# Kernel optimization log

Measured on AMD Instinct MI355X. Metric: run time of the kernel, lower is better.

Reference implementation:

```python
import jax, jax.numpy as jnp
import numpy as np

NUM_HEADS = 16
D_K = 64  # d_model // num_heads = 1024 // 16


def setup_inputs() -> dict:
    key = jax.random.key(0)
    ks = jax.random.split(key, 5)
    b, s, d = 2, 2048, 1024
    scale = 0.02
    return {
        "x": jax.random.normal(ks[0], (b, s, d), dtype=jnp.float32),
        "W_qkv": jax.random.normal(ks[1], (d, 3 * d), dtype=jnp.float32) * scale,
        "b_qkv": jax.random.normal(ks[2], (3 * d,), dtype=jnp.float32) * scale,
        "W_o": jax.random.normal(ks[3], (d, d), dtype=jnp.float32) * scale,
        "b_o": jax.random.normal(ks[4], (d,), dtype=jnp.float32) * scale,
    }


def reference(x, W_qkv, b_qkv, W_o, b_o):
    b, s, d = x.shape
    h, dk = NUM_HEADS, D_K
    # fused QKV projection: (b, s, 3*d_model)
    qkv = x @ W_qkv + b_qkv
    # faithful to the torch rearrange 'b s (h d)' with d = 3*d_k, then chunk:
    # each head's contiguous 3*d_k slice is split into q, k, v.
    qkv = qkv.reshape(b, s, h, 3 * dk).transpose(0, 2, 1, 3)  # (b, h, s, 3*dk)
    q, k, v = jnp.split(qkv, 3, axis=-1)  # each (b, h, s, dk)
    inv_scale = 1.0 / np.float32(np.sqrt(dk))
    scores = jnp.einsum("bhqd,bhkd->bhqk", q, k) * inv_scale  # (b, h, s, s)
    attn = jax.nn.softmax(scores, axis=-1)
    ctx = jnp.einsum("bhqk,bhkd->bhqd", attn, v)  # (b, h, s, dk)
    ctx = ctx.transpose(0, 2, 1, 3).reshape(b, s, d)  # (b, s, d_model)
    return ctx @ W_o + b_o
```

## Files before the change

kernel.cpp:

```cpp
#include <hip/hip_runtime.h>
#include <hip/hip_bf16.h>
#include <stdint.h>

#define NHEADS 16
#define DKH    64
#define BB     2
#define SS     2048
#define DM     1024
#define MROWS  (BB * SS)

typedef __attribute__((ext_vector_type(8))) short bf8_t;
typedef __attribute__((ext_vector_type(4))) float f4_t;
typedef unsigned short u16;
typedef uint32_t u32;

__device__ __forceinline__ u16 f2bf(float f) {
    union { float f; u32 u; } v; v.f = f;
    return (u16)((v.u + 0x7fffu + ((v.u >> 16) & 1u)) >> 16);
}

__device__ __forceinline__ float fexp2(float x) {
#if __has_builtin(__builtin_amdgcn_exp2f)
    return __builtin_amdgcn_exp2f(x);
#else
    return __expf(x * 0.69314718056f);
#endif
}

__device__ __forceinline__ void async_copy16(void* lds, const void* g) {
    __builtin_amdgcn_global_load_lds(
        (__attribute__((address_space(1))) void*)(void*)g,
        (__attribute__((address_space(3))) void*)lds, 16, 0, 0);
}

#define MFMA32(a, b, c) __builtin_amdgcn_mfma_f32_16x16x32_bf16(a, b, c, 0, 0, 0)

__global__ void k_cvt(const float* __restrict__ in, u16* __restrict__ out, int n4) {
    int stride = gridDim.x * blockDim.x;
    for (int i = blockIdx.x * blockDim.x + threadIdx.x; i < n4; i += stride) {
        float4 v = ((const float4*)in)[i];
        ushort4 o;
        o.x = f2bf(v.x); o.y = f2bf(v.y); o.z = f2bf(v.z); o.w = f2bf(v.w);
        ((ushort4*)out)[i] = o;
    }
}

__global__ void k_transpose(const float* __restrict__ W, u16* __restrict__ Wt, int K, int N) {
    __shared__ float tile[32][33];
    int n0 = blockIdx.x * 32, k0 = blockIdx.y * 32;
    int tx = threadIdx.x & 31, ty = threadIdx.x >> 5;
    #pragma unroll
    for (int r = ty; r < 32; r += 8)
        tile[r][tx] = W[(size_t)(k0 + r) * N + n0 + tx];
    __syncthreads();
    #pragma unroll
    for (int r = ty; r < 32; r += 8)
        Wt[(size_t)(n0 + r) * K + k0 + tx] = f2bf(tile[tx][r]);
}

template<int MODE>
__global__ __launch_bounds__(256) void k_gemm(
    const u16* __restrict__ A, const u16* __restrict__ Bt,
    const float* __restrict__ bias,
    u16* __restrict__ q_out, u16* __restrict__ k_out, u16* __restrict__ vt_out,
    float* __restrict__ f_out,
    int N, int K)
{
    __shared__ u16 As[128 * 32];
    __shared__ u16 Bs[128 * 32];
    const int m0 = blockIdx.y * 128, n0 = blockIdx.x * 128;
    const int tid = threadIdx.x;
    const int w = tid >> 6, l = tid & 63;
    const int lr = l >> 2, lc = (l & 3) * 8;
    const int fr = l & 15, fk = (l >> 4) * 8;
    const int wm = (w >> 1) * 64, wn = (w & 1) * 64;
    f4_t acc[4][4] = {};

    for (int kt = 0; kt < K; kt += 32) {
        #pragma unroll
        for (int cc = 0; cc < 2; ++cc) {
            const int c = w + cc * 4;
            async_copy16(As + c * 512, A  + (size_t)(m0 + c * 16 + lr) * K + kt + lc);
            async_copy16(Bs + c * 512, Bt + (size_t)(n0 + c * 16 + lr) * K + kt + lc);
        }
        __syncthreads();
        bf8_t af[4], bfr[4];
        #pragma unroll
        for (int mf = 0; mf < 4; ++mf)
            af[mf] = *(const bf8_t*)&As[(wm + mf * 16 + fr) * 32 + fk];
        #pragma unroll
        for (int nf = 0; nf < 4; ++nf)
            bfr[nf] = *(const bf8_t*)&Bs[(wn + nf * 16 + fr) * 32 + fk];
        #pragma unroll
        for (int mf = 0; mf < 4; ++mf)
            #pragma unroll
            for (int nf = 0; nf < 4; ++nf)
                acc[mf][nf] = MFMA32(af[mf], bfr[nf], acc[mf][nf]);
        __syncthreads();
    }

    #pragma unroll
    for (int mf = 0; mf < 4; ++mf)
      #pragma unroll
      for (int nf = 0; nf < 4; ++nf)
        #pragma unroll
        for (int j = 0; j < 4; ++j) {
            const int m = m0 + wm + mf * 16 + (l >> 4) * 4 + j;
            const int n = n0 + wn + nf * 16 + (l & 15);
            float v = acc[mf][nf][j] + bias[n];
            if (MODE == 0) {
                const int h = n / 192, rem = n - h * 192;
                const int which = rem >> 6, dd = rem & 63;
                const int b = m >> 11, s = m & (SS - 1);
                const u16 bv = f2bf(v);
                const size_t qk_idx = ((size_t)(b * NHEADS + h) * SS + s) * DKH + dd;
                if (which == 0)      q_out[qk_idx] = bv;
                else if (which == 1) k_out[qk_idx] = bv;
                else                 vt_out[((size_t)(b * NHEADS + h) * DKH + dd) * SS + s] = bv;
            } else {
                f_out[(size_t)m * N + n] = v;
            }
        }
}

#define SCL 0.180336880f

__global__ __launch_bounds__(256) void k_attn(
    const u16* __restrict__ Qg, const u16* __restrict__ Kg, const u16* __restrict__ Vtg,
    u16* __restrict__ ctx)
{
    __shared__ u16 Ks[64 * 64];
    __shared__ u16 Vs[64 * 64];
    const int bh = blockIdx.x;
    const int qt = blockIdx.y;
    const int tid = threadIdx.x, w = tid >> 6, l = tid & 63;
    const int fr = l & 15, fq = l >> 4;
    const int q0 = qt * 64 + w * 16;
    const u16* Qb = Qg  + (size_t)bh * SS * DKH;
    const u16* Kb = Kg  + (size_t)bh * SS * DKH;
    const u16* Vb = Vtg + (size_t)bh * DKH * SS;

    bf8_t qf[2];
    #pragma unroll
    for (int kh = 0; kh < 2; ++kh)
        qf[kh] = *(const bf8_t*)(Qb + (size_t)(q0 + fr) * DKH + kh * 32 + fq * 8);

    float mrow = -__builtin_inff(), lrow = 0.f;
    f4_t o[4] = {};

    for (int kv = 0; kv < SS; kv += 64) {
        #pragma unroll
        for (int it = 0; it < 2; ++it) {
            const int c = tid + it * 256;
            const int r = c >> 3, sl = c & 7;
            const int dsl = sl ^ (r & 7);
            *(uint4*)&Ks[r * 64 + dsl * 8] = *(const uint4*)(Kb + (size_t)(kv + r) * DKH + sl * 8);
            *(uint4*)&Vs[r * 64 + dsl * 8] = *(const uint4*)(Vb + (size_t)r * SS + kv + sl * 8);
        }
        __syncthreads();

        f4_t sa[4] = {};
        #pragma unroll
        for (int nf = 0; nf < 4; ++nf)
          #pragma unroll
          for (int kh = 0; kh < 2; ++kh) {
            const int row = nf * 16 + fr;
            const int dsl = (kh * 4 + fq) ^ (fr & 7);
            const bf8_t kb = *(const bf8_t*)&Ks[row * 64 + dsl * 8];
            sa[nf] = MFMA32(kb, qf[kh], sa[nf]);
          }

        float x = sa[0][0];
        #pragma unroll
        for (int nf = 0; nf < 4; ++nf)
          #pragma unroll
          for (int j = 0; j < 4; ++j)
            x = fmaxf(x, sa[nf][j]);
        x *= SCL;
        x = fmaxf(x, __shfl_xor(x, 16));
        x = fmaxf(x, __shfl_xor(x, 32));

        if (__any(x > mrow + 8.f)) {
            float mnew = fmaxf(mrow, x);
            float sc = fexp2(mrow - mnew);
            lrow *= sc;
            mrow = mnew;
            float sc4[4];
            #pragma unroll
            for (int j = 0; j < 4; ++j) sc4[j] = __shfl(sc, fq * 4 + j);
            #pragma unroll
            for (int df = 0; df < 4; ++df)
              #pragma unroll
              for (int j = 0; j < 4; ++j)
                o[df][j] *= sc4[j];
        }

        float ps = 0.f;
        u32 pk[8];
        #pragma unroll
        for (int nf = 0; nf < 4; ++nf) {
            float p0 = fexp2(sa[nf][0] * SCL - mrow);
            float p1 = fexp2(sa[nf][1] * SCL - mrow);
            float p2 = fexp2(sa[nf][2] * SCL - mrow);
            float p3 = fexp2(sa[nf][3] * SCL - mrow);
            ps += (p0 + p1) + (p2 + p3);
            pk[nf * 2 + 0] = ((u32)f2bf(p1) << 16) | f2bf(p0);
            pk[nf * 2 + 1] = ((u32)f2bf(p3) << 16) | f2bf(p2);
        }
        ps += __shfl_xor(ps, 16);
        ps += __shfl_xor(ps, 32);
        lrow += ps;

        union { bf8_t v; u32 u[4]; } pa[2];
        #pragma unroll
        for (int t = 0; t < 2; ++t) {
            pa[t].u[0] = pk[4 * t + 0]; pa[t].u[1] = pk[4 * t + 1];
            pa[t].u[2] = pk[4 * t + 2]; pa[t].u[3] = pk[4 * t + 3];
        }
        #pragma unroll
        for (int t = 0; t < 2; ++t) {
            const int dslA = ((4 * t)     + (fq >> 1)) ^ (fr & 7);
            const int dslB = ((4 * t + 2) + (fq >> 1)) ^ (fr & 7);
            const int hoff = (fq & 1) * 4;
            #pragma unroll
            for (int df = 0; df < 4; ++df) {
                const int row = df * 16 + fr;
                union { bf8_t v; uint2 u[2]; } vv;
                vv.u[0] = *(const uint2*)&Vs[row * 64 + dslA * 8 + hoff];
                vv.u[1] = *(const uint2*)&Vs[row * 64 + dslB * 8 + hoff];
                o[df] = MFMA32(pa[t].v, vv.v, o[df]);
            }
        }
        __syncthreads();
    }

    float ml[4];
    #pragma unroll
    for (int j = 0; j < 4; ++j) ml[j] = __shfl(lrow, fq * 4 + j);

    const int b = bh >> 4, h = bh & 15;
    #pragma unroll
    for (int df = 0; df < 4; ++df)
      #pragma unroll
      for (int j = 0; j < 4; ++j) {
        const int s = q0 + fq * 4 + j;
        const int dd = df * 16 + fr;
        float v = o[df][j] / ml[j];
        ctx[((size_t)(b * SS + s)) * DM + h * DKH + dd] = f2bf(v);
      }
}

extern "C" void kernel_launch(void* const* d_in, const int* in_sizes, int n_in,
                              void* d_out, int out_size, void* d_ws, size_t ws_size,
                              hipStream_t stream)
{
    const float* x     = (const float*)d_in[0];
    const float* W_qkv = (const float*)d_in[1];
    const float* b_qkv = (const float*)d_in[2];
    const float* W_o   = (const float*)d_in[3];
    const float* b_o   = (const float*)d_in[4];
    float* out = (float*)d_out;

    char* ws = (char*)d_ws;
    u16* xb   = (u16*)(ws);
    u16* Wqkt = (u16*)(ws + 8388608);
    u16* Wot  = (u16*)(ws + 8388608 + 6291456);
    u16* Qg   = (u16*)(ws + 16777216);
    u16* Kg   = Qg  + 4194304;
    u16* Vtg  = Kg  + 4194304;
    u16* ctx  = xb;

    k_cvt<<<1024, 256, 0, stream>>>(x, xb, (MROWS * DM) / 4);
    k_transpose<<<dim3(3 * DM / 32, DM / 32), 256, 0, stream>>>(W_qkv, Wqkt, DM, 3 * DM);
    k_transpose<<<dim3(DM / 32, DM / 32), 256, 0, stream>>>(W_o, Wot, DM, DM);
    k_gemm<0><<<dim3(3 * DM / 128, MROWS / 128), 256, 0, stream>>>(
        xb, Wqkt, b_qkv, Qg, Kg, Vtg, nullptr, 3 * DM, DM);
    k_attn<<<dim3(BB * NHEADS, SS / 64), 256, 0, stream>>>(Qg, Kg, Vtg, ctx);
    k_gemm<1><<<dim3(DM / 128, MROWS / 128), 256, 0, stream>>>(
        ctx, Wot, b_o, nullptr, nullptr, nullptr, out, DM, DM);
}
```

Baseline: 230.1 us.

## Async global-to-LDS K/V loads with permuted rows, packed bf16 convert, wide V reads

Measured after the change: 226.7 us. About the same (-1.5%).

```diff
diff --git a/kernel.cpp b/kernel.cpp
--- a/kernel.cpp
+++ b/kernel.cpp
@@ -17,6 +17,12 @@
 __device__ __forceinline__ u16 f2bf(float f) {
     union { float f; u32 u; } v; v.f = f;
     return (u16)((v.u + 0x7fffu + ((v.u >> 16) & 1u)) >> 16);
+}
+
+__device__ __forceinline__ u32 cvt_pk_bf16(float lo, float hi) {
+    u32 r;
+    asm("v_cvt_pk_bf16_f32 %0, %1, %2" : "=v"(r) : "v"(lo), "v"(hi));
+    return r;
 }
 
 __device__ __forceinline__ float fexp2(float x) {
@@ -152,10 +158,12 @@
         #pragma unroll
         for (int it = 0; it < 2; ++it) {
             const int c = tid + it * 256;
-            const int r = c >> 3, sl = c & 7;
-            const int dsl = sl ^ (r & 7);
-            *(uint4*)&Ks[r * 64 + dsl * 8] = *(const uint4*)(Kb + (size_t)(kv + r) * DKH + sl * 8);
-            *(uint4*)&Vs[r * 64 + dsl * 8] = *(const uint4*)(Vb + (size_t)r * SS + kv + sl * 8);
+            const int r = c >> 3, dslw = c & 7;
+            const int sl = dslw ^ (r & 7);
+            const int sr = ((r >> 2) & 3) * 16 + (r >> 4) * 4 + (r & 3);
+            const int cb = it * 256 + w * 64;
+            async_copy16(Ks + cb * 8, Kb + (size_t)(kv + sr) * DKH + sl * 8);
+            async_copy16(Vs + cb * 8, Vb + (size_t)r * SS + kv + sl * 8);
         }
         __syncthreads();
 
@@ -204,8 +212,8 @@
             float p2 = fexp2(sa[nf][2] * SCL - mrow);
             float p3 = fexp2(sa[nf][3] * SCL - mrow);
             ps += (p0 + p1) + (p2 + p3);
-            pk[nf * 2 + 0] = ((u32)f2bf(p1) << 16) | f2bf(p0);
-            pk[nf * 2 + 1] = ((u32)f2bf(p3) << 16) | f2bf(p2);
+            pk[nf * 2 + 0] = cvt_pk_bf16(p0, p1);
+            pk[nf * 2 + 1] = cvt_pk_bf16(p2, p3);
         }
         ps += __shfl_xor(ps, 16);
         ps += __shfl_xor(ps, 32);
@@ -219,16 +227,11 @@
         }
         #pragma unroll
         for (int t = 0; t < 2; ++t) {
-            const int dslA = ((4 * t)     + (fq >> 1)) ^ (fr & 7);
-            const int dslB = ((4 * t + 2) + (fq >> 1)) ^ (fr & 7);
-            const int hoff = (fq & 1) * 4;
+            const int dsl = (fq * 2 + t) ^ (fr & 7);
             #pragma unroll
             for (int df = 0; df < 4; ++df) {
-                const int row = df * 16 + fr;
-                union { bf8_t v; uint2 u[2]; } vv;
-                vv.u[0] = *(const uint2*)&Vs[row * 64 + dslA * 8 + hoff];
-                vv.u[1] = *(const uint2*)&Vs[row * 64 + dslB * 8 + hoff];
-                o[df] = MFMA32(pa[t].v, vv.v, o[df]);
+                const bf8_t vv = *(const bf8_t*)&Vs[(df * 16 + fr) * 64 + dsl * 8];
+                o[df] = MFMA32(pa[t].v, vv, o[df]);
             }
         }
         __syncthreads();
```
